# Kernel tuning notes

Hardware: AMD Instinct MI355X
Metric: run time of the kernel (lower is better)

Reference implementation:

```python
import jax, jax.numpy as jnp
import numpy as np

B, S, HID = 2, 2048, 4096
NH, NKV, HD = 32, 8, 128
MAX_POS = 4096
SCALE = HD ** -0.5


def _rope_tables():
    inv_freq = 1.0 / (10000.0 ** (np.arange(0, HD, 2, dtype=np.float32) / HD))
    t = np.arange(MAX_POS, dtype=np.float32)
    freqs = np.outer(t, inv_freq)              # [MAX_POS, HD/2]
    emb = np.concatenate([freqs, freqs], axis=-1)  # [MAX_POS, HD]
    return jnp.asarray(np.cos(emb)), jnp.asarray(np.sin(emb))


def setup_inputs() -> dict:
    key = jax.random.key(0)
    ks = jax.random.split(key, 6)
    hidden_states = jax.random.normal(ks[0], (B, S, HID), dtype=jnp.float32)
    position_ids = jnp.broadcast_to(jnp.arange(S, dtype=jnp.int64 if jax.config.jax_enable_x64 else jnp.int32), (B, S))
    cos_table, sin_table = _rope_tables()
    # weights stored [in, out] for x @ W
    sd = HID ** -0.5
    Wq = jax.random.normal(ks[1], (HID, NH * HD), dtype=jnp.float32) * sd
    Wk = jax.random.normal(ks[2], (HID, NKV * HD), dtype=jnp.float32) * sd
    Wv = jax.random.normal(ks[3], (HID, NKV * HD), dtype=jnp.float32) * sd
    Wo = jax.random.normal(ks[4], (NH * HD, HID), dtype=jnp.float32) * sd
    return {"hidden_states": hidden_states, "position_ids": position_ids,
            "cos_table": cos_table, "sin_table": sin_table,
            "Wq": Wq, "Wk": Wk, "Wv": Wv, "Wo": Wo}


def _rotate_half(x):
    x1, x2 = jnp.split(x, 2, axis=-1)
    return jnp.concatenate([-x2, x1], axis=-1)


def reference(hidden_states, position_ids, cos_table, sin_table, Wq, Wk, Wv, Wo):
    b, s, _ = hidden_states.shape
    q = (hidden_states @ Wq).reshape(b, s, NH, HD)
    k = (hidden_states @ Wk).reshape(b, s, NKV, HD)
    v = (hidden_states @ Wv).reshape(b, s, NKV, HD)

    # RoPE, cos/sin gathered by position and unsqueezed at head dim (dim=2, bsnd)
    cos = cos_table[position_ids][:, :, None, :]  # [b, s, 1, hd]
    sin = sin_table[position_ids][:, :, None, :]
    q = q * cos + _rotate_half(q) * sin
    k = k * cos + _rotate_half(k) * sin

    # GQA: expand kv heads to match query heads
    rep = NH // NKV
    k = jnp.repeat(k, rep, axis=2)  # [b, s, NH, hd]
    v = jnp.repeat(v, rep, axis=2)

    scores = jnp.einsum('bqnd,bknd->bnqk', q, k) * SCALE  # [b, NH, s, s]
    causal = jnp.tril(jnp.ones((s, s), dtype=bool))
    scores = jnp.where(causal, scores, jnp.finfo(scores.dtype).min)
    probs = jax.nn.softmax(scores, axis=-1)
    attn = jnp.einsum('bnqk,bknd->bqnd', probs, v)  # [b, s, NH, hd]
    attn = attn.reshape(b, s, NH * HD)
    return attn @ Wo
```

## Files before the change

kernel.cpp:

```cpp
#include <hip/hip_runtime.h>
#include <stdint.h>

typedef unsigned short u16;
typedef __bf16 bf16x8 __attribute__((ext_vector_type(8)));
typedef unsigned short u16x8 __attribute__((ext_vector_type(8)));
typedef unsigned short u16x4 __attribute__((ext_vector_type(4)));
typedef float f32x4 __attribute__((ext_vector_type(4)));

#define B_ 2
#define S_ 2048
#define HID_ 4096
#define NH_ 32
#define NKV_ 8
#define HD_ 128
#define NTOT_ 6144
#define SCALE_ 0.08838834764831845f

#define GLD16(gp, lp)                                                     \
  __builtin_amdgcn_global_load_lds(                                       \
      (__attribute__((address_space(1))) void*)(gp),                      \
      (__attribute__((address_space(3))) void*)(lp), 16, 0, 0)

__device__ __forceinline__ u16 f2b(float f) {
  union { float f; uint32_t u; } v; v.f = f;
  uint32_t u = v.u;
  u = u + 0x7fffu + ((u >> 16) & 1u);
  return (u16)(u >> 16);
}
__device__ __forceinline__ float b2f(u16 s) {
  union { uint32_t u; float f; } v; v.u = ((uint32_t)s) << 16;
  return v.f;
}
__device__ __forceinline__ bf16x8 ldb8(const u16* p) {
  u16x8 u = *(const u16x8*)p;
  return __builtin_bit_cast(bf16x8, u);
}
__device__ __forceinline__ bf16x8 ldb8b(const char* p) {
  u16x8 u = *(const u16x8*)p;
  return __builtin_bit_cast(bf16x8, u);
}

__global__ __launch_bounds__(256) void k_convx(const float* __restrict__ src,
                                               u16* __restrict__ dst, int n4) {
  int i = blockIdx.x * 256 + threadIdx.x;
  if (i >= n4) return;
  const float4 v = ((const float4*)src)[i];
  u16x4 o = { f2b(v.x), f2b(v.y), f2b(v.z), f2b(v.w) };
  *(u16x4*)(dst + (size_t)i * 4) = o;
}

__global__ __launch_bounds__(256) void k_convT(const float* __restrict__ src,
                                               u16* __restrict__ dst, int N, int Kd) {
  __shared__ u16 tile[64][65];
  int k0 = blockIdx.x * 64, n0 = blockIdx.y * 64;
  int t = threadIdx.x;
  int rr = t >> 4;
  int cc = (t & 15) * 4;
#pragma unroll
  for (int p = 0; p < 4; ++p) {
    int r = p * 16 + rr;
    float4 v = *(const float4*)&src[(size_t)(k0 + r) * N + n0 + cc];
    tile[cc + 0][r] = f2b(v.x);
    tile[cc + 1][r] = f2b(v.y);
    tile[cc + 2][r] = f2b(v.z);
    tile[cc + 3][r] = f2b(v.w);
  }
  __syncthreads();
#pragma unroll
  for (int p = 0; p < 4; ++p) {
    int n = p * 16 + rr;
    u16x4 o = { tile[n][cc], tile[n][cc + 1], tile[n][cc + 2], tile[n][cc + 3] };
    *(u16x4*)&dst[(size_t)(n0 + n) * Kd + k0 + cc] = o;
  }
}

template <int MODE>
__global__ __launch_bounds__(512, 2) void k_gemm(const u16* __restrict__ A,
                                                 const u16* __restrict__ Bt,
                                                 float* __restrict__ Cf,
                                                 u16* __restrict__ Qb,
                                                 u16* __restrict__ Kb,
                                                 u16* __restrict__ Vb,
                                                 int M, int N, int Kd) {
  __shared__ __align__(16) char smem[131072];
  const int NT = Kd >> 5;

  int nwg = gridDim.x * gridDim.y;
  int orig = blockIdx.y * gridDim.x + blockIdx.x;
  int cpx = nwg >> 3;
  int swz = (orig & 7) * cpx + (orig >> 3);
  int bx = swz % gridDim.x, by = swz / gridDim.x;
  int m0 = by * 256, n0 = bx * 256;

  int t = threadIdx.x, lane = t & 63, wave = t >> 6;
  int wr = wave >> 2, wc = wave & 3;
  int lg = lane >> 4, l16 = lane & 15;
  int loff = l16 * 64 + ((lg ^ ((l16 >> 1) & 3)) << 4);

  int srow = lane >> 2;
  int schk = (lane & 3) ^ ((lane >> 3) & 3);
  const u16* sA0 = A  + (size_t)(m0 + wave * 16 + srow) * Kd + schk * 8;
  const u16* sA1 = sA0 + (size_t)128 * Kd;
  const u16* sB0 = Bt + (size_t)(n0 + wave * 16 + srow) * Kd + schk * 8;
  const u16* sB1 = sB0 + (size_t)128 * Kd;

  f32x4 acc[8][4] = {};

#define STAGE_A(kt) do { char* dst_ = smem + ((kt) & 3) * 32768 + wave * 1024;          \
    GLD16(sA0 + (size_t)(kt) * 32, dst_); GLD16(sA1 + (size_t)(kt) * 32, dst_ + 8192); } while (0)
#define STAGE_B(kt) do { char* dst_ = smem + ((kt) & 3) * 32768 + 16384 + wave * 1024;  \
    GLD16(sB0 + (size_t)(kt) * 32, dst_); GLD16(sB1 + (size_t)(kt) * 32, dst_ + 8192); } while (0)

  STAGE_A(0); STAGE_B(0);
  STAGE_A(1); STAGE_B(1);
  STAGE_A(2); STAGE_B(2);
  asm volatile("s_waitcnt vmcnt(8)" ::: "memory");
  __syncthreads();

  for (int kt = 0; kt < NT; ++kt) {
    char* Ab = smem + (kt & 3) * 32768;
    char* Bb = Ab + 16384;
    bf16x8 bfr[4], af[4];
#pragma unroll
    for (int j = 0; j < 4; ++j) bfr[j] = ldb8b(Bb + (wc * 4 + j) * 1024 + loff);
#pragma unroll
    for (int i = 0; i < 4; ++i) af[i] = ldb8b(Ab + (wr * 8 + i) * 1024 + loff);
    if (kt + 3 < NT) STAGE_A(kt + 3);
    __builtin_amdgcn_s_setprio(1);
#pragma unroll
    for (int i = 0; i < 4; ++i)
#pragma unroll
      for (int j = 0; j < 4; ++j)
        acc[i][j] = __builtin_amdgcn_mfma_f32_16x16x32_bf16(af[i], bfr[j], acc[i][j], 0, 0, 0);
    __builtin_amdgcn_s_setprio(0);
#pragma unroll
    for (int i = 0; i < 4; ++i) af[i] = ldb8b(Ab + (wr * 8 + 4 + i) * 1024 + loff);
    if (kt + 3 < NT) STAGE_B(kt + 3);
    __builtin_amdgcn_s_setprio(1);
#pragma unroll
    for (int i = 0; i < 4; ++i)
#pragma unroll
      for (int j = 0; j < 4; ++j)
        acc[4 + i][j] = __builtin_amdgcn_mfma_f32_16x16x32_bf16(af[i], bfr[j], acc[4 + i][j], 0, 0, 0);
    __builtin_amdgcn_s_setprio(0);
    if (kt < NT - 3) {
      asm volatile("s_waitcnt vmcnt(8)" ::: "memory");
      __syncthreads();
    } else if (kt == NT - 3) {
      asm volatile("s_waitcnt vmcnt(4)" ::: "memory");
      __syncthreads();
    } else if (kt == NT - 2) {
      asm volatile("s_waitcnt vmcnt(0)" ::: "memory");
      __syncthreads();
    }
  }
#undef STAGE_A
#undef STAGE_B

  if (MODE == 1) {
#pragma unroll
    for (int i = 0; i < 8; ++i)
#pragma unroll
      for (int j = 0; j < 4; ++j)
#pragma unroll
        for (int r = 0; r < 4; ++r) {
          int m = m0 + wr * 128 + i * 16 + lg * 4 + r;
          int n = n0 + wc * 64 + j * 16 + l16;
          Cf[(size_t)m * N + n] = acc[i][j][r];
        }
  } else {
    int slice = (n0 >> 7) + (wc >> 1);
#pragma unroll
    for (int i = 0; i < 8; ++i)
#pragma unroll
      for (int j = 0; j < 4; ++j)
#pragma unroll
        for (int r = 0; r < 4; ++r) {
          int m = m0 + wr * 128 + i * 16 + lg * 4 + r;
          int d = ((wc & 1) << 6) + j * 16 + l16;
          int b = m >> 11, s = m & (S_ - 1);
          u16 val = f2b(acc[i][j][r]);
          if (slice < NH_) {
            Qb[(((size_t)b * NH_ + slice) * S_ + s) * HD_ + d] = val;
          } else if (slice < NH_ + NKV_) {
            Kb[(((size_t)b * NKV_ + (slice - NH_)) * S_ + s) * HD_ + d] = val;
          } else {
            Vb[(((size_t)b * NKV_ + (slice - NH_ - NKV_)) * HD_ + d) * S_ + s] = val;
          }
        }
  }
}

__global__ __launch_bounds__(256) void k_rope(u16* __restrict__ buf, const int* __restrict__ pos,
                                              const float* __restrict__ ct, const float* __restrict__ st,
                                              int H, int rows) {
  int wave = threadIdx.x >> 6, lane = threadIdx.x & 63;
  int row = blockIdx.x * 4 + wave;
  if (row >= rows) return;
  int s = row & (S_ - 1);
  int b = row / (H * S_);
  int p = pos[b * S_ + s];
  size_t base = (size_t)row * HD_;
  float x1 = b2f(buf[base + lane]);
  float x2 = b2f(buf[base + 64 + lane]);
  float c  = ct[(size_t)p * HD_ + lane];
  float sn = st[(size_t)p * HD_ + lane];
  buf[base + lane]      = f2b(x1 * c - x2 * sn);
  buf[base + 64 + lane] = f2b(x2 * c + x1 * sn);
}

__global__ __launch_bounds__(256, 4) void k_attn(const u16* __restrict__ Q,
                                                 const u16* __restrict__ K,
                                                 const u16* __restrict__ Vt,
                                                 u16* __restrict__ Ob) {
  __shared__ __align__(16) char smem[40960];
  const int VS_OFF = 16384, PS_OFF = 32768;

  int bid = blockIdx.x;
  int pid = bid & 15;
  int h   = (bid >> 4) & 31;
  int b   = bid >> 9;
  int kvh = h >> 2;
  int tid = threadIdx.x;
  int wave = tid >> 6, lane = tid & 63;
  int lg = lane >> 4, l16 = lane & 15;
  int lsw = (l16 & 7) << 4;

  const u16* Qp = Q  + (((size_t)b * NH_  + h)   * S_) * HD_;
  const u16* Kp = K  + (((size_t)b * NKV_ + kvh) * S_) * HD_;
  const u16* Vp = Vt + (((size_t)b * NKV_ + kvh) * HD_) * S_;

  for (int pass = 0; pass < 2; ++pass) {
    int qt = pass ? (31 - pid) : pid;
    int q0 = qt * 64 + wave * 16;
    int qg = q0 + l16;

    bf16x8 qf[4];
#pragma unroll
    for (int c = 0; c < 4; ++c)
      qf[c] = ldb8(&Qp[(size_t)qg * HD_ + c * 32 + lg * 8]);

    f32x4 oacc[8] = {};
    float mrun = -1e30f, lrun = 0.f;

    int nt = qt + 1;
    for (int tI = 0; tI < nt; ++tI) {
      int kb = tI * 64;
      __syncthreads();
#pragma unroll
      for (int i = 0; i < 4; ++i) {
        int ci = i * 256 + tid;
        int r = ci >> 4, ch = ci & 15;
        u16x8 v = *(const u16x8*)&Kp[(size_t)(kb + r) * HD_ + ch * 8];
        *(u16x8*)(smem + r * 256 + ((ch * 16) ^ ((r & 7) << 4))) = v;
      }
#pragma unroll
      for (int i = 0; i < 4; ++i) {
        int ci = i * 256 + tid;
        int r = ci >> 3, ch = ci & 7;
        u16x8 v = *(const u16x8*)&Vp[(size_t)r * S_ + kb + ch * 8];
        *(u16x8*)(smem + VS_OFF + r * 128 + ((ch * 16) ^ ((r & 7) << 4))) = v;
      }
      __syncthreads();

      f32x4 sc[4] = {};
#pragma unroll
      for (int c = 0; c < 4; ++c) {
#pragma unroll
        for (int n = 0; n < 4; ++n) {
          bf16x8 kf = ldb8b(smem + (n * 16 + l16) * 256 + ((c * 64 + lg * 16) ^ lsw));
          sc[n] = __builtin_amdgcn_mfma_f32_16x16x32_bf16(kf, qf[c], sc[n], 0, 0, 0);
        }
      }

      bool diag = (tI == qt);
      float mx = -1e30f;
#pragma unroll
      for (int n = 0; n < 4; ++n)
#pragma unroll
        for (int r = 0; r < 4; ++r) {
          float v = sc[n][r];
          int key = kb + n * 16 + lg * 4 + r;
          if (diag && key > qg) v = -1e30f;
          sc[n][r] = v;
          mx = fmaxf(mx, v);
        }
      mx = fmaxf(mx, __shfl_xor(mx, 16));
      mx = fmaxf(mx, __shfl_xor(mx, 32));
      float mnew = fmaxf(mrun, mx * SCALE_);
      float alpha = __expf(mrun - mnew);
      float ps = 0.f;
#pragma unroll
      for (int n = 0; n < 4; ++n) {
        u16x4 pk;
#pragma unroll
        for (int r = 0; r < 4; ++r) {
          float p = __expf(fmaf(sc[n][r], SCALE_, -mnew));
          ps += p;
          pk[r] = f2b(p);
        }
        *(u16x4*)(smem + PS_OFF + wave * 2048 + l16 * 128 + ((n * 32 + lg * 8) ^ lsw)) = pk;
      }
      ps += __shfl_xor(ps, 16);
      ps += __shfl_xor(ps, 32);
      lrun = lrun * alpha + ps;
      mrun = mnew;

      float ar[4];
#pragma unroll
      for (int r = 0; r < 4; ++r) ar[r] = __shfl(alpha, lg * 4 + r);
#pragma unroll
      for (int ns = 0; ns < 8; ++ns)
#pragma unroll
        for (int r = 0; r < 4; ++r) oacc[ns][r] *= ar[r];

#pragma unroll
      for (int ck = 0; ck < 2; ++ck) {
        bf16x8 pa = ldb8b(smem + PS_OFF + wave * 2048 + l16 * 128 + ((ck * 64 + lg * 16) ^ lsw));
#pragma unroll
        for (int ns = 0; ns < 8; ++ns) {
          bf16x8 vf = ldb8b(smem + VS_OFF + (ns * 16 + l16) * 128 + ((ck * 64 + lg * 16) ^ lsw));
          oacc[ns] = __builtin_amdgcn_mfma_f32_16x16x32_bf16(pa, vf, oacc[ns], 0, 0, 0);
        }
      }
    }

    float lr[4];
#pragma unroll
    for (int r = 0; r < 4; ++r) lr[r] = 1.0f / __shfl(lrun, lg * 4 + r);
#pragma unroll
    for (int ns = 0; ns < 8; ++ns)
#pragma unroll
      for (int r = 0; r < 4; ++r) {
        int q = q0 + lg * 4 + r;
        Ob[((size_t)(b * S_) + q) * (NH_ * HD_) + h * HD_ + ns * 16 + l16] =
            f2b(oacc[ns][r] * lr[r]);
      }
  }
}

extern "C" void kernel_launch(void* const* d_in, const int* in_sizes, int n_in,
                              void* d_out, int out_size, void* d_ws, size_t ws_size,
                              hipStream_t stream) {
  const float* hs  = (const float*)d_in[0];
  const int*   pos = (const int*)d_in[1];
  const float* ct  = (const float*)d_in[2];
  const float* st  = (const float*)d_in[3];
  const float* Wq  = (const float*)d_in[4];
  const float* Wk  = (const float*)d_in[5];
  const float* Wv  = (const float*)d_in[6];
  const float* Wo  = (const float*)d_in[7];
  float* out = (float*)d_out;

  char* w = (char*)d_ws;
  u16* Xb    = (u16*)(w);
  u16* WqkvT = (u16*)(w + 33554432ull);
  u16* WoT   = (u16*)(w + 83886080ull);
  u16* Qb    = (u16*)(w + 117440512ull);
  u16* Kb    = (u16*)(w + 150994944ull);
  u16* Vb    = (u16*)(w + 159383552ull);
  u16* Attb  = (u16*)(w + 167772160ull);

  k_convx<<<16384, 256, 0, stream>>>(hs, Xb, 4194304);
  k_convT<<<dim3(64, 64), 256, 0, stream>>>(Wq, WqkvT, 4096, 4096);
  k_convT<<<dim3(64, 16), 256, 0, stream>>>(Wk, WqkvT + (size_t)4096 * 4096, 1024, 4096);
  k_convT<<<dim3(64, 16), 256, 0, stream>>>(Wv, WqkvT + (size_t)5120 * 4096, 1024, 4096);
  k_convT<<<dim3(64, 64), 256, 0, stream>>>(Wo, WoT, 4096, 4096);
  k_gemm<0><<<dim3(24, 16), 512, 0, stream>>>(Xb, WqkvT, nullptr, Qb, Kb, Vb, 4096, NTOT_, 4096);
  k_rope<<<32768, 256, 0, stream>>>(Qb, pos, ct, st, NH_, B_ * NH_ * S_);
  k_rope<<<8192, 256, 0, stream>>>(Kb, pos, ct, st, NKV_, B_ * NKV_ * S_);
  k_attn<<<1024, 256, 0, stream>>>(Qb, Kb, Vb, Attb);
  k_gemm<1><<<dim3(16, 16), 512, 0, stream>>>(Attb, WoT, out, nullptr, nullptr, nullptr, 4096, 4096, 4096);
}
```

Before: 670.0 us.

## Restructure GEMM pipeline to double-buffered 64-wide K tiles with split barriers

The GEMM main loop moves from a 4-stage ring of 32-wide K slices to two buffers of 64-wide K tiles, with each tile split into two 32-wide chunks. Loads for the next tile are issued per chunk and interleaved with the MFMA blocks, using raw s_barrier calls in place of full __syncthreads. The global-to-LDS staging layout also changes: each wave now loads a 32-row block. The goal is fewer loop iterations and better overlap of memory traffic with MFMA work. The risks are a shallower prefetch depth and more barriers per iteration. The kernel is also split into two non-template entry points wrapping a shared device body.

```diff
diff --git a/kernel.cpp b/kernel.cpp
--- a/kernel.cpp
+++ b/kernel.cpp
@@ -75,15 +75,15 @@
 }
 
 template <int MODE>
-__global__ __launch_bounds__(512, 2) void k_gemm(const u16* __restrict__ A,
-                                                 const u16* __restrict__ Bt,
-                                                 float* __restrict__ Cf,
-                                                 u16* __restrict__ Qb,
-                                                 u16* __restrict__ Kb,
-                                                 u16* __restrict__ Vb,
-                                                 int M, int N, int Kd) {
+__device__ __forceinline__ void gemm_body(const u16* __restrict__ A,
+                                          const u16* __restrict__ Bt,
+                                          float* __restrict__ Cf,
+                                          u16* __restrict__ Qb,
+                                          u16* __restrict__ Kb,
+                                          u16* __restrict__ Vb,
+                                          int M, int N, int Kd) {
   __shared__ __align__(16) char smem[131072];
-  const int NT = Kd >> 5;
+  const int NT = Kd >> 6;
 
   int nwg = gridDim.x * gridDim.y;
   int orig = blockIdx.y * gridDim.x + blockIdx.x;
@@ -96,36 +96,38 @@
   int wr = wave >> 2, wc = wave & 3;
   int lg = lane >> 4, l16 = lane & 15;
   int loff = l16 * 64 + ((lg ^ ((l16 >> 1) & 3)) << 4);
-
-  int srow = lane >> 2;
-  int schk = (lane & 3) ^ ((lane >> 3) & 3);
-  const u16* sA0 = A  + (size_t)(m0 + wave * 16 + srow) * Kd + schk * 8;
-  const u16* sA1 = sA0 + (size_t)128 * Kd;
-  const u16* sB0 = Bt + (size_t)(n0 + wave * 16 + srow) * Kd + schk * 8;
-  const u16* sB1 = sB0 + (size_t)128 * Kd;
+  int srow = lane >> 2, schk = (lane & 3) ^ ((lane >> 3) & 3);
+
+  const u16* Asrc = A  + (size_t)(m0 + wave * 32 + srow) * Kd + schk * 8;
+  const u16* Bsrc = Bt + (size_t)(n0 + wave * 32 + srow) * Kd + schk * 8;
 
   f32x4 acc[8][4] = {};
 
-#define STAGE_A(kt) do { char* dst_ = smem + ((kt) & 3) * 32768 + wave * 1024;          \
-    GLD16(sA0 + (size_t)(kt) * 32, dst_); GLD16(sA1 + (size_t)(kt) * 32, dst_ + 8192); } while (0)
-#define STAGE_B(kt) do { char* dst_ = smem + ((kt) & 3) * 32768 + 16384 + wave * 1024;  \
-    GLD16(sB0 + (size_t)(kt) * 32, dst_); GLD16(sB1 + (size_t)(kt) * 32, dst_ + 8192); } while (0)
-
-  STAGE_A(0); STAGE_B(0);
-  STAGE_A(1); STAGE_B(1);
-  STAGE_A(2); STAGE_B(2);
-  asm volatile("s_waitcnt vmcnt(8)" ::: "memory");
+#define STG_A(kt, kc) do {                                                          \
+    char* d_ = smem + (((kt) & 1) << 16) + ((kc) << 14) + (wave << 11);             \
+    const u16* s_ = Asrc + (size_t)(kt) * 64 + (kc) * 32;                           \
+    GLD16(s_, d_); GLD16(s_ + (size_t)16 * Kd, d_ + 1024); } while (0)
+#define STG_B(kt, kc) do {                                                          \
+    char* d_ = smem + (((kt) & 1) << 16) + 32768 + ((kc) << 14) + (wave << 11);     \
+    const u16* s_ = Bsrc + (size_t)(kt) * 64 + (kc) * 32;                           \
+    GLD16(s_, d_); GLD16(s_ + (size_t)16 * Kd, d_ + 1024); } while (0)
+
+  STG_A(0, 0); STG_B(0, 0); STG_A(0, 1); STG_B(0, 1);
+  asm volatile("s_waitcnt vmcnt(0)" ::: "memory");
   __syncthreads();
 
   for (int kt = 0; kt < NT; ++kt) {
-    char* Ab = smem + (kt & 3) * 32768;
-    char* Bb = Ab + 16384;
+    const char* bufA = smem + ((kt & 1) << 16);
+    const char* bufB = bufA + 32768;
+    bool pf = (kt + 1 < NT);
     bf16x8 bfr[4], af[4];
-#pragma unroll
-    for (int j = 0; j < 4; ++j) bfr[j] = ldb8b(Bb + (wc * 4 + j) * 1024 + loff);
-#pragma unroll
-    for (int i = 0; i < 4; ++i) af[i] = ldb8b(Ab + (wr * 8 + i) * 1024 + loff);
-    if (kt + 3 < NT) STAGE_A(kt + 3);
+
+#pragma unroll
+    for (int j = 0; j < 4; ++j) bfr[j] = ldb8b(bufB + ((wc * 4 + j) << 10) + loff);
+#pragma unroll
+    for (int i = 0; i < 4; ++i) af[i] = ldb8b(bufA + ((wr * 8 + i) << 10) + loff);
+    if (pf) STG_A(kt + 1, 0);
+    __builtin_amdgcn_s_barrier();
     __builtin_amdgcn_s_setprio(1);
 #pragma unroll
     for (int i = 0; i < 4; ++i)
@@ -133,9 +135,12 @@
       for (int j = 0; j < 4; ++j)
         acc[i][j] = __builtin_amdgcn_mfma_f32_16x16x32_bf16(af[i], bfr[j], acc[i][j], 0, 0, 0);
     __builtin_amdgcn_s_setprio(0);
-#pragma unroll
-    for (int i = 0; i < 4; ++i) af[i] = ldb8b(Ab + (wr * 8 + 4 + i) * 1024 + loff);
-    if (kt + 3 < NT) STAGE_B(kt + 3);
+    __builtin_amdgcn_s_barrier();
+
+#pragma unroll
+    for (int i = 0; i < 4; ++i) af[i] = ldb8b(bufA + ((wr * 8 + 4 + i) << 10) + loff);
+    if (pf) STG_B(kt + 1, 0);
+    __builtin_amdgcn_s_barrier();
     __builtin_amdgcn_s_setprio(1);
 #pragma unroll
     for (int i = 0; i < 4; ++i)
@@ -143,19 +148,40 @@
       for (int j = 0; j < 4; ++j)
         acc[4 + i][j] = __builtin_amdgcn_mfma_f32_16x16x32_bf16(af[i], bfr[j], acc[4 + i][j], 0, 0, 0);
     __builtin_amdgcn_s_setprio(0);
-    if (kt < NT - 3) {
-      asm volatile("s_waitcnt vmcnt(8)" ::: "memory");
-      __syncthreads();
-    } else if (kt == NT - 3) {
-      asm volatile("s_waitcnt vmcnt(4)" ::: "memory");
-      __syncthreads();
-    } else if (kt == NT - 2) {
-      asm volatile("s_waitcnt vmcnt(0)" ::: "memory");
-      __syncthreads();
-    }
+    asm volatile("s_waitcnt vmcnt(4)" ::: "memory");
+    __builtin_amdgcn_s_barrier();
+
+#pragma unroll
+    for (int j = 0; j < 4; ++j) bfr[j] = ldb8b(bufB + 16384 + ((wc * 4 + j) << 10) + loff);
+#pragma unroll
+    for (int i = 0; i < 4; ++i) af[i] = ldb8b(bufA + 16384 + ((wr * 8 + i) << 10) + loff);
+    if (pf) STG_A(kt + 1, 1);
+    __builtin_amdgcn_s_barrier();
+    __builtin_amdgcn_s_setprio(1);
+#pragma unroll
+    for (int i = 0; i < 4; ++i)
+#pragma unroll
+      for (int j = 0; j < 4; ++j)
+        acc[i][j] = __builtin_amdgcn_mfma_f32_16x16x32_bf16(af[i], bfr[j], acc[i][j], 0, 0, 0);
+    __builtin_amdgcn_s_setprio(0);
+    __builtin_amdgcn_s_barrier();
+
+#pragma unroll
+    for (int i = 0; i < 4; ++i) af[i] = ldb8b(bufA + 16384 + ((wr * 8 + 4 + i) << 10) + loff);
+    if (pf) STG_B(kt + 1, 1);
+    __builtin_amdgcn_s_barrier();
+    __builtin_amdgcn_s_setprio(1);
+#pragma unroll
+    for (int i = 0; i < 4; ++i)
+#pragma unroll
+      for (int j = 0; j < 4; ++j)
+        acc[4 + i][j] = __builtin_amdgcn_mfma_f32_16x16x32_bf16(af[i], bfr[j], acc[4 + i][j], 0, 0, 0);
+    __builtin_amdgcn_s_setprio(0);
+    asm volatile("s_waitcnt vmcnt(4)" ::: "memory");
+    __builtin_amdgcn_s_barrier();
   }
-#undef STAGE_A
-#undef STAGE_B
+#undef STG_A
+#undef STG_B
 
   if (MODE == 1) {
 #pragma unroll
@@ -189,6 +215,22 @@
           }
         }
   }
+}
+
+__global__ __launch_bounds__(512, 2) void k_gemm_qkv(const u16* __restrict__ A,
+                                                     const u16* __restrict__ Bt,
+                                                     u16* __restrict__ Qb,
+                                                     u16* __restrict__ Kb,
+                                                     u16* __restrict__ Vb,
+                                                     int M, int N, int Kd) {
+  gemm_body<0>(A, Bt, nullptr, Qb, Kb, Vb, M, N, Kd);
+}
+
+__global__ __launch_bounds__(512, 2) void k_gemm_out(const u16* __restrict__ A,
+                                                     const u16* __restrict__ Bt,
+                                                     float* __restrict__ Cf,
+                                                     int M, int N, int Kd) {
+  gemm_body<1>(A, Bt, Cf, nullptr, nullptr, nullptr, M, N, Kd);
 }
 
 __global__ __launch_bounds__(256) void k_rope(u16* __restrict__ buf, const int* __restrict__ pos,
@@ -366,9 +408,9 @@
   k_convT<<<dim3(64, 16), 256, 0, stream>>>(Wk, WqkvT + (size_t)4096 * 4096, 1024, 4096);
   k_convT<<<dim3(64, 16), 256, 0, stream>>>(Wv, WqkvT + (size_t)5120 * 4096, 1024, 4096);
   k_convT<<<dim3(64, 64), 256, 0, stream>>>(Wo, WoT, 4096, 4096);
-  k_gemm<0><<<dim3(24, 16), 512, 0, stream>>>(Xb, WqkvT, nullptr, Qb, Kb, Vb, 4096, NTOT_, 4096);
+  k_gemm_qkv<<<dim3(24, 16), 512, 0, stream>>>(Xb, WqkvT, Qb, Kb, Vb, 4096, NTOT_, 4096);
   k_rope<<<32768, 256, 0, stream>>>(Qb, pos, ct, st, NH_, B_ * NH_ * S_);
   k_rope<<<8192, 256, 0, stream>>>(Kb, pos, ct, st, NKV_, B_ * NKV_ * S_);
   k_attn<<<1024, 256, 0, stream>>>(Qb, Kb, Vb, Attb);
-  k_gemm<1><<<dim3(16, 16), 512, 0, stream>>>(Attb, WoT, out, nullptr, nullptr, nullptr, 4096, 4096, 4096);
-}
+  k_gemm_out<<<dim3(16, 16), 512, 0, stream>>>(Attb, WoT, out, 4096, 4096, 4096);
+}
```

Measured after the change: 636.8 us. 4.9% less time.
